# Kernel tuning notes

Hardware: AMD Instinct MI355X
Metric: run time of the kernel (lower is better)

## Reference

```python
import jax, jax.numpy as jnp
import numpy as np

B, S, D = 1, 2048, 2048
H, KV, HD = 32, 8, 64
POWER = 100000.0


def _rotary(x):
    # x: [B, h, S, HD]; faithful to RotaryEncoder: freqs = pos / div_term
    rot_dim = HD // 2
    pos = jnp.arange(S, dtype=x.dtype)
    div = POWER ** (jnp.arange(0, HD, 2, dtype=x.dtype) / HD)  # [HD//2]
    freqs = pos[:, None] / div  # [S, HD//2]
    cos, sin = jnp.cos(freqs), jnp.sin(freqs)
    x_rot, x_pass = x[..., :rot_dim], x[..., rot_dim:]
    h = rot_dim // 2
    rot_half = jnp.concatenate([-x_rot[..., h:], x_rot[..., :h]], axis=-1)
    return jnp.concatenate([x_rot * cos + rot_half * sin, x_pass], axis=-1)


def setup_inputs() -> dict:
    key = jax.random.key(0)
    k1, k2, k3 = jax.random.split(key, 3)
    hidden_states = jax.random.normal(k1, (B, S, D), dtype=jnp.float32)
    op_size = H * HD + 2 * KV * HD
    Wqkv = jax.random.normal(k2, (D, op_size), dtype=jnp.float32) * 0.02
    Wo = jax.random.normal(k3, (H * HD, D), dtype=jnp.float32) * 0.02
    causal = jnp.tril(jnp.ones((S, S), dtype=bool))
    attention_mask = jnp.where(causal, 0.0, -1e9).astype(jnp.float32)[None, None]
    return {"hidden_states": hidden_states, "attention_mask": attention_mask,
            "Wqkv": Wqkv, "Wo": Wo}


def reference(hidden_states, attention_mask, Wqkv, Wo):
    groups = H // KV
    qkv = hidden_states @ Wqkv  # [B, S, op_size]
    qpos = H * HD
    q = qkv[..., :qpos].reshape(B, S, H, HD).transpose(0, 2, 1, 3)
    k = qkv[..., qpos:qpos + KV * HD].reshape(B, S, KV, HD).transpose(0, 2, 1, 3)
    v = qkv[..., qpos + KV * HD:].reshape(B, S, KV, HD).transpose(0, 2, 1, 3)
    q = _rotary(q)
    k = _rotary(k)
    k = jnp.repeat(k, groups, axis=1)  # GQA repeat_interleave -> [B, H, S, HD]
    v = jnp.repeat(v, groups, axis=1)
    scores = jnp.einsum('bhqd,bhkd->bhqk', q, k) / jnp.sqrt(jnp.float32(HD))
    scores = scores + attention_mask[..., :S]
    attn = jax.nn.softmax(scores.astype(jnp.float32), axis=-1).astype(v.dtype)
    out = jnp.einsum('bhqk,bhkd->bhqd', attn, v)
    out = out.transpose(0, 2, 1, 3).reshape(B, S, H * HD)
    return out @ Wo
```

## Files before the change

kernel.cpp:

```cpp
#include <hip/hip_runtime.h>
#include <hip/hip_bf16.h>
#include <cstdint>
#include <cstddef>

#define S_LEN 2048
#define D_MODEL 2048
#define NH 32
#define NKV 8
#define HDIM 64
#define OPSZ 3072
#define KOFF 2048
#define VOFF 2560

typedef float    floatx4 __attribute__((ext_vector_type(4)));
typedef __bf16   bf16x8  __attribute__((ext_vector_type(8)));
typedef __bf16   bf16x4  __attribute__((ext_vector_type(4)));
typedef __bf16   bf16_t;
typedef _Float16 f16_t;
typedef _Float16 f16x2   __attribute__((ext_vector_type(2)));
typedef _Float16 f16x4   __attribute__((ext_vector_type(4)));
typedef _Float16 f16x8   __attribute__((ext_vector_type(8)));
typedef __fp16   hfx2    __attribute__((ext_vector_type(2)));

__device__ __forceinline__ void gld16(const void* g, void* l) {
  __builtin_amdgcn_global_load_lds((__attribute__((address_space(1))) void*)(void*)g,
                                   (__attribute__((address_space(3))) void*)l,
                                   16, 0, 0);
}

__global__ __launch_bounds__(256)
void prep_kernel(const float* __restrict__ X, const float* __restrict__ Wqkv,
                 const float* __restrict__ Wo, bf16_t* __restrict__ Xb,
                 bf16_t* __restrict__ WqkvT, bf16_t* __restrict__ WoT) {
  const int bx = blockIdx.x;
  const int k0 = blockIdx.y * 32;
  const int tx = threadIdx.x & 31, ty = threadIdx.x >> 5;
  if (bx < 160) {
    __shared__ float tile[32][33];
    const float* W; bf16_t* Wt; int N, n0;
    if (bx < 96) { W = Wqkv; Wt = WqkvT; N = OPSZ;    n0 = bx * 32; }
    else         { W = Wo;   Wt = WoT;   N = D_MODEL; n0 = (bx - 96) * 32; }
#pragma unroll
    for (int i = 0; i < 32; i += 8)
      tile[ty + i][tx] = W[(size_t)(k0 + ty + i) * N + n0 + tx];
    __syncthreads();
#pragma unroll
    for (int i = 0; i < 32; i += 8)
      Wt[(size_t)(n0 + ty + i) * D_MODEL + k0 + tx] = (bf16_t)tile[tx][ty + i];
  } else {
    const int n0 = (bx - 160) * 32;
#pragma unroll
    for (int i = 0; i < 32; i += 8) {
      const size_t idx = (size_t)(k0 + ty + i) * D_MODEL + n0 + tx;
      Xb[idx] = (bf16_t)X[idx];
    }
  }
}

#define GEMM128_CORE(A_, Bt_, K_, m0_, n0_)                                       \
  const int tid = threadIdx.x;                                                    \
  const int wave = tid >> 6;                                                      \
  const int lane = tid & 63;                                                      \
  const int lane15 = lane & 15;                                                   \
  const int quad = lane >> 4;                                                     \
  const int wm = (wave & 1) * 64;                                                 \
  const int wn = (wave >> 1) * 64;                                                \
  floatx4 acc[4][4];                                                              \
  _Pragma("unroll") for (int i = 0; i < 4; i++)                                   \
    _Pragma("unroll") for (int j = 0; j < 4; j++)                                 \
      acc[i][j] = floatx4{0.f, 0.f, 0.f, 0.f};                                    \
  {                                                                               \
      \
      \
    int srow[4], scol[4];                                                         \
    _Pragma("unroll") for (int i = 0; i < 4; i++) {                               \
      const int c = tid + i * 256;                                                \
      srow[i] = c >> 3;                                                           \
      scol[i] = (((c & 7) * 16) ^ ((srow[i] & 7) << 4)) >> 1;                     \
    }                                                                             \
    const bf16_t* Ab = (A_) + (size_t)(m0_) * (K_);                               \
    const bf16_t* Bb = (Bt_) + (size_t)(n0_) * (K_);                              \
    const int rsw = (lane15 & 7) << 4;         \
    for (int k0 = 0; k0 < (K_); k0 += 64) {                                       \
      __syncthreads();                                                            \
      _Pragma("unroll") for (int i = 0; i < 4; i++)                               \
        gld16(Ab + (size_t)srow[i] * (K_) + k0 + scol[i],                         \
              &As[(i * 256 + wave * 64) * 8]);                                    \
      _Pragma("unroll") for (int i = 0; i < 4; i++)                               \
        gld16(Bb + (size_t)srow[i] * (K_) + k0 + scol[i],                         \
              &Bs[(i * 256 + wave * 64) * 8]);                                    \
      __syncthreads();                                                            \
      _Pragma("unroll") for (int kt = 0; kt < 2; kt++) {                          \
        const int off = ((kt * 64 + quad * 16) ^ rsw) >> 1;                       \
        bf16x8 af[4], bfr[4];                                                     \
        _Pragma("unroll") for (int mi = 0; mi < 4; mi++)                          \
          af[mi] = *(const bf16x8*)&As[(wm + mi * 16 + lane15) * 64 + off];       \
        _Pragma("unroll") for (int ni = 0; ni < 4; ni++)                          \
          bfr[ni] = *(const bf16x8*)&Bs[(wn + ni * 16 + lane15) * 64 + off];      \
        _Pragma("unroll") for (int mi = 0; mi < 4; mi++)                          \
          _Pragma("unroll") for (int ni = 0; ni < 4; ni++)                        \
            acc[mi][ni] = __builtin_amdgcn_mfma_f32_16x16x32_bf16(af[mi], bfr[ni],\
                                                                  acc[mi][ni], 0, 0, 0); \
      }                                                                           \
    }                                                                             \
  }

#define XCD_SWZ(m0_, n0_)                                                         \
  const int gx_ = gridDim.x;                                                      \
  const int id_ = blockIdx.y * gx_ + blockIdx.x;                                  \
  const int cpx_ = (gx_ * gridDim.y) >> 3;                                        \
  const int sid_ = (id_ & 7) * cpx_ + (id_ >> 3);                                 \
  const int m0_ = (sid_ / gx_) * 128;                                             \
  const int n0_ = (sid_ % gx_) * 128;

#define QSCALE 0.18033688011112042f
__global__ __launch_bounds__(256, 3)
void gemm_qkv_rope(const bf16_t* __restrict__ A, const bf16_t* __restrict__ Bt,
                   bf16_t* __restrict__ Qr, bf16_t* __restrict__ Kr,
                   f16_t* __restrict__ VtG) {
  __shared__ bf16_t As[128 * 64];
  __shared__ bf16_t Bs[128 * 64];
  XCD_SWZ(m0, n0)
  GEMM128_CORE(A, Bt, D_MODEL, m0, n0)

  const int colbase = n0 + wn;
  const int s0 = m0 + wm;

  if (colbase < VOFF) {
    const bool isQ = (colbase < KOFF);
    const float k2 = 0.51905126483f;
    const float pj0 = exp2f(-(float)lane15 * k2);
    const float pj1 = pj0 * 0.0031622776601684f;
    bf16_t* dst = isQ ? (Qr + ((size_t)(colbase >> 6) * S_LEN) * HDIM)
                      : (Kr + ((size_t)((colbase - KOFF) >> 6) * S_LEN) * HDIM);
    const float qs = isQ ? QSCALE : 1.0f;
#pragma unroll
    for (int mi = 0; mi < 4; mi++) {
#pragma unroll
      for (int r = 0; r < 4; r++) {
        const int s = s0 + mi * 16 + quad * 4 + r;
        const float sf = (float)s;
        float s0s, s0c, s1s, s1c;
        __sincosf(sf * pj0, &s0s, &s0c);
        __sincosf(sf * pj1, &s1s, &s1c);
        const float x0 = acc[mi][0][r], x1 = acc[mi][1][r];
        bf16_t* row = dst + (size_t)s * HDIM + lane15;
        row[0]  = (bf16_t)((x0 * s0c - x1 * s0s) * qs);
        row[16] = (bf16_t)((x1 * s1c + x0 * s1s) * qs);
        row[32] = (bf16_t)(acc[mi][2][r] * qs);
        row[48] = (bf16_t)(acc[mi][3][r] * qs);
      }
    }
  } else {
    const int kvv = (colbase - VOFF) >> 6;
    f16_t* dst = VtG + (size_t)kvv * HDIM * S_LEN;
#pragma unroll
    for (int mi = 0; mi < 4; mi++) {
      const int s = s0 + mi * 16 + quad * 4;
#pragma unroll
      for (int ni = 0; ni < 4; ni++) {
        const int d = ni * 16 + lane15;
        f16x4 tv;
#pragma unroll
        for (int r = 0; r < 4; r++) tv[r] = (f16_t)acc[mi][ni][r];
        *(f16x4*)&dst[(size_t)d * S_LEN + s] = tv;
      }
    }
  }
}

__global__ __launch_bounds__(256, 3)
void gemm_bt_f32out(const bf16_t* __restrict__ A, const bf16_t* __restrict__ Bt,
                    float* __restrict__ C, int M, int N, int K) {
  __shared__ bf16_t As[128 * 64];
  __shared__ bf16_t Bs[128 * 64];
  XCD_SWZ(m0, n0)
  GEMM128_CORE(A, Bt, K, m0, n0)

#pragma unroll
  for (int mi = 0; mi < 4; mi++)
#pragma unroll
    for (int r = 0; r < 4; r++) {
      const int row = m0 + wm + mi * 16 + quad * 4 + r;
#pragma unroll
      for (int ni = 0; ni < 4; ni++) {
        const int col = n0 + wn + ni * 16 + lane15;
        C[(size_t)row * N + col] = acc[mi][ni][r];
      }
    }
}

__global__ __launch_bounds__(256, 4)
void flash_kernel(const bf16_t* __restrict__ Qr, const bf16_t* __restrict__ Kr,
                  const f16_t* __restrict__ VtG, bf16_t* __restrict__ attn) {
  __shared__ bf16_t Ks[128 * 64];
  __shared__ f16_t  Vt[64 * 128];

  const int tid = threadIdx.x;
  const int wave = tid >> 6;
  const int lane = tid & 63;
  const int lane15 = lane & 15;
  const int quad = lane >> 4;
  const int bx = blockIdx.x;
  const int h = bx & 31;
  const int qblk = 31 - (bx >> 5);
  const int q0 = qblk * 64;
  const int rq = q0 + wave * 16;
  const int kv = h >> 2;
  const size_t kbase = (size_t)kv * S_LEN * HDIM;
  const size_t vbase = (size_t)kv * HDIM * S_LEN;

  const int krow0 = tid >> 3;
  const int kcol  = ((((tid & 7) * 16) ^ ((krow0 & 7) << 4)) >> 1);
  const int vd0   = tid >> 4;
  const int vcol  = ((((tid & 15) * 16) ^ ((vd0 & 15) << 4)) >> 1);

  const int kswz = (lane15 & 7) << 4;
  const int vswz = lane15 << 4;

  bf16x8 aq[2];
#pragma unroll
  for (int kt = 0; kt < 2; kt++)
    aq[kt] = *(const bf16x8*)&Qr[((size_t)h * S_LEN + rq + lane15) * HDIM + kt * 32 + quad * 8];

  const f16x4 vone = {(f16_t)1.0f, (f16_t)1.0f, (f16_t)1.0f, (f16_t)1.0f};

  float m_run = -1e30f;
  floatx4 lacc = floatx4{0.f, 0.f, 0.f, 0.f};
  floatx4 o[4];
#pragma unroll
  for (int dt = 0; dt < 4; dt++) o[dt] = floatx4{0.f, 0.f, 0.f, 0.f};

  const int nk = (qblk + 2) >> 1;

  for (int t = 0; t < nk; ++t) {
    const int p0 = t * 128;
    __syncthreads();
#pragma unroll
    for (int i = 0; i < 4; i++)
      gld16(Kr + kbase + (size_t)(p0 + krow0 + i * 32) * HDIM + kcol,
            &Ks[(i * 256 + wave * 64) * 8]);
#pragma unroll
    for (int i = 0; i < 4; i++)
      gld16(VtG + vbase + (size_t)(vd0 + i * 16) * S_LEN + p0 + vcol,
            &Vt[(i * 256 + wave * 64) * 8]);
    __syncthreads();

    floatx4 sc[8];
#pragma unroll
    for (int nt = 0; nt < 8; nt++) sc[nt] = floatx4{0.f, 0.f, 0.f, 0.f};
#pragma unroll
    for (int kt = 0; kt < 2; kt++) {
#pragma unroll
      for (int nt = 0; nt < 8; nt++) {
        const bf16x8 ak = *(const bf16x8*)&Ks[(nt * 16 + lane15) * 64 +
                                              (((kt * 64 + quad * 16) ^ kswz) >> 1)];
        sc[nt] = __builtin_amdgcn_mfma_f32_16x16x32_bf16(ak, aq[kt], sc[nt], 0, 0, 0);
      }
    }

    if (p0 + 127 > rq) {
#pragma unroll
      for (int nt = 0; nt < 8; nt++)
#pragma unroll
        for (int r = 0; r < 4; r++) {
          const int kpos = p0 + nt * 16 + quad * 4 + r;
          const int qrow = rq + lane15;
          if (kpos > qrow) sc[nt][r] = -1e30f;
        }
    }

    float mt = -1e30f;
#pragma unroll
    for (int nt = 0; nt < 8; nt++) {
      mt = fmaxf(fmaxf(mt, sc[nt][0]), sc[nt][1]);
      mt = fmaxf(fmaxf(mt, sc[nt][2]), sc[nt][3]);
    }
    mt = fmaxf(mt, __shfl_xor(mt, 16));
    mt = fmaxf(mt, __shfl_xor(mt, 32));
    const float mnew = fmaxf(m_run, mt);
    const float alpha = __builtin_amdgcn_exp2f(m_run - mnew);
    m_run = mnew;

    f16x4 ph[8];
#pragma unroll
    for (int nt = 0; nt < 8; nt++) {
      const float e0 = __builtin_amdgcn_exp2f(sc[nt][0] - mnew);
      const float e1 = __builtin_amdgcn_exp2f(sc[nt][1] - mnew);
      const float e2 = __builtin_amdgcn_exp2f(sc[nt][2] - mnew);
      const float e3 = __builtin_amdgcn_exp2f(sc[nt][3] - mnew);
      const hfx2 lo_ = __builtin_amdgcn_cvt_pkrtz(e0, e1);
      const hfx2 hi_ = __builtin_amdgcn_cvt_pkrtz(e2, e3);
      const f16x2 lo = __builtin_bit_cast(f16x2, lo_);
      const f16x2 hi = __builtin_bit_cast(f16x2, hi_);
      ph[nt] = __builtin_shufflevector(lo, hi, 0, 1, 2, 3);
    }

    lacc = lacc * alpha;
#pragma unroll
    for (int dt = 0; dt < 4; dt++) o[dt] = o[dt] * alpha;

#pragma unroll
    for (int kt4 = 0; kt4 < 8; kt4++) {
      lacc = __builtin_amdgcn_mfma_f32_16x16x16f16(vone, ph[kt4], lacc, 0, 0, 0);
#pragma unroll
      for (int dt = 0; dt < 4; dt++) {
        const f16x4 av = *(const f16x4*)&Vt[(dt * 16 + lane15) * 128 +
                                            (((kt4 * 32 + quad * 8) ^ vswz) >> 1)];
        o[dt] = __builtin_amdgcn_mfma_f32_16x16x16f16(av, ph[kt4], o[dt], 0, 0, 0);
      }
    }
  }

  const float inv = 1.0f / lacc[0];
  const int s = rq + lane15;
#pragma unroll
  for (int dt = 0; dt < 4; dt++) {
    bf16x4 tv;
#pragma unroll
    for (int r = 0; r < 4; r++) tv[r] = (bf16_t)(o[dt][r] * inv);
    *(bf16x4*)&attn[(size_t)s * D_MODEL + h * HDIM + dt * 16 + quad * 4] = tv;
  }
}

extern "C" void kernel_launch(void* const* d_in, const int* in_sizes, int n_in,
                              void* d_out, int out_size, void* d_ws, size_t ws_size,
                              hipStream_t stream) {
  (void)in_sizes; (void)n_in; (void)out_size; (void)ws_size;
  const float* hidden = (const float*)d_in[0];
  const float* Wqkv = (const float*)d_in[2];
  const float* Wo   = (const float*)d_in[3];
  float* out = (float*)d_out;

  char* ws = (char*)d_ws;
  size_t off = 0;
  auto alloc = [&](size_t bytes) -> void* {
    void* p = ws + off;
    off += (bytes + 255) & ~(size_t)255;
    return p;
  };
  bf16_t* Xb    = (bf16_t*)alloc((size_t)S_LEN * D_MODEL * 2);
  bf16_t* WqkvT = (bf16_t*)alloc((size_t)OPSZ * D_MODEL * 2);
  bf16_t* WoT   = (bf16_t*)alloc((size_t)D_MODEL * D_MODEL * 2);
  bf16_t* Qr    = (bf16_t*)alloc((size_t)NH * S_LEN * HDIM * 2);
  bf16_t* Kr    = (bf16_t*)alloc((size_t)NKV * S_LEN * HDIM * 2);
  f16_t*  VtG   = (f16_t*) alloc((size_t)NKV * HDIM * S_LEN * 2);
  bf16_t* attn  = (bf16_t*)alloc((size_t)S_LEN * D_MODEL * 2);

  prep_kernel<<<dim3(224, 64), 256, 0, stream>>>(hidden, Wqkv, Wo, Xb, WqkvT, WoT);
  gemm_qkv_rope<<<dim3(OPSZ / 128, S_LEN / 128), 256, 0, stream>>>(Xb, WqkvT, Qr, Kr, VtG);
  flash_kernel<<<dim3(32 * NH), 256, 0, stream>>>(Qr, Kr, VtG, attn);
  gemm_bt_f32out<<<dim3(D_MODEL / 128, S_LEN / 128), 256, 0, stream>>>(attn, WoT, out, S_LEN, D_MODEL, D_MODEL);
}
```

Before: 213.7 us.

## Double-buffer GEMM LDS tiles and enlarge flash-attention query block to 128 rows

The shared GEMM core now uses two LDS buffers per operand, issuing global-to-LDS loads for the next k-tile while the current one is computed, with explicit vmcnt waits and barriers replacing the two syncthreads per iteration. The flash kernel processes 128 query rows per block (32 per wave, two 16-row fragments), so each K/V tile loaded into LDS is reused by twice as many queries and half as many blocks are launched. Occupancy targets drop to 2 blocks per CU to cover the doubled LDS and larger register footprint. The risk is less latency hiding from lower occupancy and coarser causal load balance across fewer attention blocks.

New measurement: 209.8 us. About the same (-1.8%).

```diff
diff --git a/kernel.cpp b/kernel.cpp
--- a/kernel.cpp
+++ b/kernel.cpp
@@ -27,6 +27,13 @@
                                    (__attribute__((address_space(3))) void*)l,
                                    16, 0, 0);
 }
+
+#define ACQ(N) do { asm volatile("s_waitcnt vmcnt(" #N ")" ::: "memory");        \
+                    __builtin_amdgcn_s_barrier();                                \
+                    __builtin_amdgcn_sched_barrier(0); } while (0)
+#define REL()  do { __builtin_amdgcn_sched_barrier(0);                           \
+                    __builtin_amdgcn_s_barrier();                                \
+                    __builtin_amdgcn_sched_barrier(0); } while (0)
 
 __global__ __launch_bounds__(256)
 void prep_kernel(const float* __restrict__ X, const float* __restrict__ Wqkv,
@@ -70,8 +77,6 @@
     _Pragma("unroll") for (int j = 0; j < 4; j++)                                 \
       acc[i][j] = floatx4{0.f, 0.f, 0.f, 0.f};                                    \
   {                                                                               \
-      \
-      \
     int srow[4], scol[4];                                                         \
     _Pragma("unroll") for (int i = 0; i < 4; i++) {                               \
       const int c = tid + i * 256;                                                \
@@ -80,30 +85,53 @@
     }                                                                             \
     const bf16_t* Ab = (A_) + (size_t)(m0_) * (K_);                               \
     const bf16_t* Bb = (Bt_) + (size_t)(n0_) * (K_);                              \
-    const int rsw = (lane15 & 7) << 4;         \
-    for (int k0 = 0; k0 < (K_); k0 += 64) {                                       \
-      __syncthreads();                                                            \
+    const int rsw = (lane15 & 7) << 4;                                            \
+    auto stage = [&](bf16_t* dA, bf16_t* dB, int k0) {                            \
       _Pragma("unroll") for (int i = 0; i < 4; i++)                               \
         gld16(Ab + (size_t)srow[i] * (K_) + k0 + scol[i],                         \
-              &As[(i * 256 + wave * 64) * 8]);                                    \
+              dA + (i * 256 + wave * 64) * 8);                                    \
       _Pragma("unroll") for (int i = 0; i < 4; i++)                               \
         gld16(Bb + (size_t)srow[i] * (K_) + k0 + scol[i],                         \
-              &Bs[(i * 256 + wave * 64) * 8]);                                    \
-      __syncthreads();                                                            \
+              dB + (i * 256 + wave * 64) * 8);                                    \
+    };                                                                            \
+    auto comp = [&](const bf16_t* sA, const bf16_t* sB) {                         \
       _Pragma("unroll") for (int kt = 0; kt < 2; kt++) {                          \
         const int off = ((kt * 64 + quad * 16) ^ rsw) >> 1;                       \
         bf16x8 af[4], bfr[4];                                                     \
         _Pragma("unroll") for (int mi = 0; mi < 4; mi++)                          \
-          af[mi] = *(const bf16x8*)&As[(wm + mi * 16 + lane15) * 64 + off];       \
+          af[mi] = *(const bf16x8*)&sA[(wm + mi * 16 + lane15) * 64 + off];       \
         _Pragma("unroll") for (int ni = 0; ni < 4; ni++)                          \
-          bfr[ni] = *(const bf16x8*)&Bs[(wn + ni * 16 + lane15) * 64 + off];      \
+          bfr[ni] = *(const bf16x8*)&sB[(wn + ni * 16 + lane15) * 64 + off];      \
         _Pragma("unroll") for (int mi = 0; mi < 4; mi++)                          \
           _Pragma("unroll") for (int ni = 0; ni < 4; ni++)                        \
             acc[mi][ni] = __builtin_amdgcn_mfma_f32_16x16x32_bf16(af[mi], bfr[ni],\
                                                                   acc[mi][ni], 0, 0, 0); \
       }                                                                           \
+    };                                                                            \
+    const int NT = (K_) / 64;                                                     \
+    stage(As0, Bs0, 0);                                                           \
+    stage(As1, Bs1, 64);                                                          \
+    for (int t = 0; t < NT - 2; t += 2) {                                         \
+      ACQ(8);                                                                     \
+      comp(As0, Bs0);                                                             \
+      REL();                                                                      \
+      stage(As0, Bs0, (t + 2) * 64);                                              \
+      ACQ(8);                                                                     \
+      comp(As1, Bs1);                                                             \
+      REL();                                                                      \
+      stage(As1, Bs1, (t + 3) * 64);                                              \
     }                                                                             \
-  }
+    ACQ(8);                                                                       \
+    comp(As0, Bs0);                                                               \
+    ACQ(0);                                                                       \
+    comp(As1, Bs1);                                                               \
+  }
+
+#define GEMM128_LDS                                                               \
+  __shared__ bf16_t As0[128 * 64];                                                \
+  __shared__ bf16_t As1[128 * 64];                                                \
+  __shared__ bf16_t Bs0[128 * 64];                                                \
+  __shared__ bf16_t Bs1[128 * 64];
 
 #define XCD_SWZ(m0_, n0_)                                                         \
   const int gx_ = gridDim.x;                                                      \
@@ -114,12 +142,11 @@
   const int n0_ = (sid_ % gx_) * 128;
 
 #define QSCALE 0.18033688011112042f
-__global__ __launch_bounds__(256, 3)
+__global__ __launch_bounds__(256, 2)
 void gemm_qkv_rope(const bf16_t* __restrict__ A, const bf16_t* __restrict__ Bt,
                    bf16_t* __restrict__ Qr, bf16_t* __restrict__ Kr,
                    f16_t* __restrict__ VtG) {
-  __shared__ bf16_t As[128 * 64];
-  __shared__ bf16_t Bs[128 * 64];
+  GEMM128_LDS
   XCD_SWZ(m0, n0)
   GEMM128_CORE(A, Bt, D_MODEL, m0, n0)
 
@@ -169,11 +196,10 @@
   }
 }
 
-__global__ __launch_bounds__(256, 3)
+__global__ __launch_bounds__(256, 2)
 void gemm_bt_f32out(const bf16_t* __restrict__ A, const bf16_t* __restrict__ Bt,
                     float* __restrict__ C, int M, int N, int K) {
-  __shared__ bf16_t As[128 * 64];
-  __shared__ bf16_t Bs[128 * 64];
+  GEMM128_LDS
   XCD_SWZ(m0, n0)
   GEMM128_CORE(A, Bt, K, m0, n0)
 
@@ -190,7 +216,7 @@
     }
 }
 
-__global__ __launch_bounds__(256, 4)
+__global__ __launch_bounds__(256, 2)
 void flash_kernel(const bf16_t* __restrict__ Qr, const bf16_t* __restrict__ Kr,
                   const f16_t* __restrict__ VtG, bf16_t* __restrict__ attn) {
   __shared__ bf16_t Ks[128 * 64];
@@ -203,9 +229,9 @@
   const int quad = lane >> 4;
   const int bx = blockIdx.x;
   const int h = bx & 31;
-  const int qblk = 31 - (bx >> 5);
-  const int q0 = qblk * 64;
-  const int rq = q0 + wave * 16;
+  const int qblk = 15 - (bx >> 5);
+  const int q0 = qblk * 128;
+  const int rq = q0 + wave * 32;
   const int kv = h >> 2;
   const size_t kbase = (size_t)kv * S_LEN * HDIM;
   const size_t vbase = (size_t)kv * HDIM * S_LEN;
@@ -218,20 +244,25 @@
   const int kswz = (lane15 & 7) << 4;
   const int vswz = lane15 << 4;
 
-  bf16x8 aq[2];
-#pragma unroll
-  for (int kt = 0; kt < 2; kt++)
-    aq[kt] = *(const bf16x8*)&Qr[((size_t)h * S_LEN + rq + lane15) * HDIM + kt * 32 + quad * 8];
+  bf16x8 aq[2][2];
+#pragma unroll
+  for (int f = 0; f < 2; f++)
+#pragma unroll
+    for (int kt = 0; kt < 2; kt++)
+      aq[f][kt] = *(const bf16x8*)&Qr[((size_t)h * S_LEN + rq + f * 16 + lane15) * HDIM +
+                                      kt * 32 + quad * 8];
 
   const f16x4 vone = {(f16_t)1.0f, (f16_t)1.0f, (f16_t)1.0f, (f16_t)1.0f};
 
-  float m_run = -1e30f;
-  floatx4 lacc = floatx4{0.f, 0.f, 0.f, 0.f};
-  floatx4 o[4];
-#pragma unroll
-  for (int dt = 0; dt < 4; dt++) o[dt] = floatx4{0.f, 0.f, 0.f, 0.f};
-
-  const int nk = (qblk + 2) >> 1;
+  float m_run[2] = {-1e30f, -1e30f};
+  floatx4 lacc[2] = {floatx4{0.f, 0.f, 0.f, 0.f}, floatx4{0.f, 0.f, 0.f, 0.f}};
+  floatx4 o[2][4];
+#pragma unroll
+  for (int f = 0; f < 2; f++)
+#pragma unroll
+    for (int dt = 0; dt < 4; dt++) o[f][dt] = floatx4{0.f, 0.f, 0.f, 0.f};
+
+  const int nk = qblk + 1;
 
   for (int t = 0; t < nk; ++t) {
     const int p0 = t * 128;
@@ -246,80 +277,91 @@
             &Vt[(i * 256 + wave * 64) * 8]);
     __syncthreads();
 
-    floatx4 sc[8];
-#pragma unroll
-    for (int nt = 0; nt < 8; nt++) sc[nt] = floatx4{0.f, 0.f, 0.f, 0.f};
+    floatx4 sc[2][8];
+#pragma unroll
+    for (int f = 0; f < 2; f++)
+#pragma unroll
+      for (int nt = 0; nt < 8; nt++) sc[f][nt] = floatx4{0.f, 0.f, 0.f, 0.f};
 #pragma unroll
     for (int kt = 0; kt < 2; kt++) {
 #pragma unroll
       for (int nt = 0; nt < 8; nt++) {
         const bf16x8 ak = *(const bf16x8*)&Ks[(nt * 16 + lane15) * 64 +
                                               (((kt * 64 + quad * 16) ^ kswz) >> 1)];
-        sc[nt] = __builtin_amdgcn_mfma_f32_16x16x32_bf16(ak, aq[kt], sc[nt], 0, 0, 0);
-      }
-    }
-
-    if (p0 + 127 > rq) {
-#pragma unroll
-      for (int nt = 0; nt < 8; nt++)
-#pragma unroll
-        for (int r = 0; r < 4; r++) {
-          const int kpos = p0 + nt * 16 + quad * 4 + r;
-          const int qrow = rq + lane15;
-          if (kpos > qrow) sc[nt][r] = -1e30f;
-        }
-    }
-
-    float mt = -1e30f;
-#pragma unroll
-    for (int nt = 0; nt < 8; nt++) {
-      mt = fmaxf(fmaxf(mt, sc[nt][0]), sc[nt][1]);
-      mt = fmaxf(fmaxf(mt, sc[nt][2]), sc[nt][3]);
-    }
-    mt = fmaxf(mt, __shfl_xor(mt, 16));
-    mt = fmaxf(mt, __shfl_xor(mt, 32));
-    const float mnew = fmaxf(m_run, mt);
-    const float alpha = __builtin_amdgcn_exp2f(m_run - mnew);
-    m_run = mnew;
-
-    f16x4 ph[8];
-#pragma unroll
-    for (int nt = 0; nt < 8; nt++) {
-      const float e0 = __builtin_amdgcn_exp2f(sc[nt][0] - mnew);
-      const float e1 = __builtin_amdgcn_exp2f(sc[nt][1] - mnew);
-      const float e2 = __builtin_amdgcn_exp2f(sc[nt][2] - mnew);
-      const float e3 = __builtin_amdgcn_exp2f(sc[nt][3] - mnew);
-      const hfx2 lo_ = __builtin_amdgcn_cvt_pkrtz(e0, e1);
-      const hfx2 hi_ = __builtin_amdgcn_cvt_pkrtz(e2, e3);
-      const f16x2 lo = __builtin_bit_cast(f16x2, lo_);
-      const f16x2 hi = __builtin_bit_cast(f16x2, hi_);
-      ph[nt] = __builtin_shufflevector(lo, hi, 0, 1, 2, 3);
-    }
-
-    lacc = lacc * alpha;
-#pragma unroll
-    for (int dt = 0; dt < 4; dt++) o[dt] = o[dt] * alpha;
+        sc[0][nt] = __builtin_amdgcn_mfma_f32_16x16x32_bf16(ak, aq[0][kt], sc[0][nt], 0, 0, 0);
+        sc[1][nt] = __builtin_amdgcn_mfma_f32_16x16x32_bf16(ak, aq[1][kt], sc[1][nt], 0, 0, 0);
+      }
+    }
+
+    f16x4 ph[2][8];
+#pragma unroll
+    for (int f = 0; f < 2; f++) {
+      if (p0 + 127 > rq + f * 16) {
+#pragma unroll
+        for (int nt = 0; nt < 8; nt++)
+#pragma unroll
+          for (int r = 0; r < 4; r++) {
+            const int kpos = p0 + nt * 16 + quad * 4 + r;
+            const int qrow = rq + f * 16 + lane15;
+            if (kpos > qrow) sc[f][nt][r] = -1e30f;
+          }
+      }
+
+      float mt = -1e30f;
+#pragma unroll
+      for (int nt = 0; nt < 8; nt++) {
+        mt = fmaxf(fmaxf(mt, sc[f][nt][0]), sc[f][nt][1]);
+        mt = fmaxf(fmaxf(mt, sc[f][nt][2]), sc[f][nt][3]);
+      }
+      mt = fmaxf(mt, __shfl_xor(mt, 16));
+      mt = fmaxf(mt, __shfl_xor(mt, 32));
+      const float mnew = fmaxf(m_run[f], mt);
+      const float alpha = __builtin_amdgcn_exp2f(m_run[f] - mnew);
+      m_run[f] = mnew;
+
+#pragma unroll
+      for (int nt = 0; nt < 8; nt++) {
+        const float e0 = __builtin_amdgcn_exp2f(sc[f][nt][0] - mnew);
+        const float e1 = __builtin_amdgcn_exp2f(sc[f][nt][1] - mnew);
+        const float e2 = __builtin_amdgcn_exp2f(sc[f][nt][2] - mnew);
+        const float e3 = __builtin_amdgcn_exp2f(sc[f][nt][3] - mnew);
+        const hfx2 lo_ = __builtin_amdgcn_cvt_pkrtz(e0, e1);
+        const hfx2 hi_ = __builtin_amdgcn_cvt_pkrtz(e2, e3);
+        const f16x2 lo = __builtin_bit_cast(f16x2, lo_);
+        const f16x2 hi = __builtin_bit_cast(f16x2, hi_);
+        ph[f][nt] = __builtin_shufflevector(lo, hi, 0, 1, 2, 3);
+      }
+
+      lacc[f] = lacc[f] * alpha;
+#pragma unroll
+      for (int dt = 0; dt < 4; dt++) o[f][dt] = o[f][dt] * alpha;
+    }
 
 #pragma unroll
     for (int kt4 = 0; kt4 < 8; kt4++) {
-      lacc = __builtin_amdgcn_mfma_f32_16x16x16f16(vone, ph[kt4], lacc, 0, 0, 0);
+      lacc[0] = __builtin_amdgcn_mfma_f32_16x16x16f16(vone, ph[0][kt4], lacc[0], 0, 0, 0);
+      lacc[1] = __builtin_amdgcn_mfma_f32_16x16x16f16(vone, ph[1][kt4], lacc[1], 0, 0, 0);
 #pragma unroll
       for (int dt = 0; dt < 4; dt++) {
         const f16x4 av = *(const f16x4*)&Vt[(dt * 16 + lane15) * 128 +
                                             (((kt4 * 32 + quad * 8) ^ vswz) >> 1)];
-        o[dt] = __builtin_amdgcn_mfma_f32_16x16x16f16(av, ph[kt4], o[dt], 0, 0, 0);
-      }
-    }
-  }
-
-  const float inv = 1.0f / lacc[0];
-  const int s = rq + lane15;
-#pragma unroll
-  for (int dt = 0; dt < 4; dt++) {
-    bf16x4 tv;
-#pragma unroll
-    for (int r = 0; r < 4; r++) tv[r] = (bf16_t)(o[dt][r] * inv);
-    *(bf16x4*)&attn[(size_t)s * D_MODEL + h * HDIM + dt * 16 + quad * 4] = tv;
+        o[0][dt] = __builtin_amdgcn_mfma_f32_16x16x16f16(av, ph[0][kt4], o[0][dt], 0, 0, 0);
+        o[1][dt] = __builtin_amdgcn_mfma_f32_16x16x16f16(av, ph[1][kt4], o[1][dt], 0, 0, 0);
+      }
+    }
+  }
+
+#pragma unroll
+  for (int f = 0; f < 2; f++) {
+    const float inv = 1.0f / lacc[f][0];
+    const int s = rq + f * 16 + lane15;
+#pragma unroll
+    for (int dt = 0; dt < 4; dt++) {
+      bf16x4 tv;
+#pragma unroll
+      for (int r = 0; r < 4; r++) tv[r] = (bf16_t)(o[f][dt][r] * inv);
+      *(bf16x4*)&attn[(size_t)s * D_MODEL + h * HDIM + dt * 16 + quad * 4] = tv;
+    }
   }
 }
 
@@ -349,6 +391,6 @@
 
   prep_kernel<<<dim3(224, 64), 256, 0, stream>>>(hidden, Wqkv, Wo, Xb, WqkvT, WoT);
   gemm_qkv_rope<<<dim3(OPSZ / 128, S_LEN / 128), 256, 0, stream>>>(Xb, WqkvT, Qr, Kr, VtG);
-  flash_kernel<<<dim3(32 * NH), 256, 0, stream>>>(Qr, Kr, VtG, attn);
+  flash_kernel<<<dim3(16 * NH), 256, 0, stream>>>(Qr, Kr, VtG, attn);
   gemm_bt_f32out<<<dim3(D_MODEL / 128, S_LEN / 128), 256, 0, stream>>>(attn, WoT, out, S_LEN, D_MODEL, D_MODEL);
 }
```
